# Kernel tuning notes

Hardware: AMD Instinct MI355X
Metric: run time of the kernel (lower is better)

Reference implementation:

```python
import jax, jax.numpy as jnp
import numpy as np


def _prelu(x, a):
    return jnp.where(x >= 0, x, a * x)


def _conv1x1(x, w, b, a):
    # x: [N,C,H,W], w: [O,C], b: [O] -> PReLU(conv1x1(x))
    y = jnp.einsum('oc,nchw->nohw', w, x) + b[None, :, None, None]
    return _prelu(y, a)


def setup_inputs() -> dict:
    key = jax.random.key(0)
    ks = jax.random.split(key, 8)
    N, C, H, W = 4, 128, 64, 64
    Cr = C // 2  # reduction=2
    sC = 1.0 / np.sqrt(C)
    x = jax.random.normal(ks[0], (N, C, H, W), dtype=jnp.float32)
    w1 = jax.random.normal(ks[1], (Cr, C), dtype=jnp.float32) * sC
    b1 = jnp.zeros((Cr,), dtype=jnp.float32)
    a1 = jnp.asarray(0.25, dtype=jnp.float32)  # PReLU (single shared slope)
    w2 = jax.random.normal(ks[2], (Cr, C), dtype=jnp.float32) * sC
    b2 = jnp.zeros((Cr,), dtype=jnp.float32)
    a2 = jnp.asarray(0.25, dtype=jnp.float32)
    wa = jax.random.normal(ks[3], (C, C), dtype=jnp.float32) * sC
    ba = jnp.zeros((C,), dtype=jnp.float32)
    aa = jnp.asarray(0.25, dtype=jnp.float32)
    return {"x": x, "w1": w1, "b1": b1, "a1": a1,
            "w2": w2, "b2": b2, "a2": a2,
            "wa": wa, "ba": ba, "aa": aa}


def reference(x, w1, b1, a1, w2, b2, a2, wa, ba, aa):
    N, C, H, W = x.shape
    HW = H * W
    e1 = _conv1x1(x, w1, b1, a1).reshape(N, -1, HW)   # [N,Cr,HW]
    e2 = _conv1x1(x, w2, b2, a2).reshape(N, -1, HW)   # [N,Cr,HW]
    asm = _conv1x1(x, wa, ba, aa).reshape(N, C, HW)   # [N,C,HW]
    # ksize=1: per-channel outer products summed over channels == single contraction
    score = jnp.einsum('nci,ncj->nij', e1, e2)        # [N,HW,HW]
    score = jax.nn.softmax(score, axis=2)
    out = jnp.einsum('nij,ncj->nci', score, asm)      # [N,C,HW]
    return out.reshape(N, C, H, W)
```

## Files before the change

kernel.cpp:

```cpp
#include <hip/hip_runtime.h>
#include <hip/hip_bf16.h>
#include <stdint.h>


typedef float   f32x16 __attribute__((ext_vector_type(16)));
typedef __bf16  bf16x8 __attribute__((ext_vector_type(8)));
typedef __bf16  bf16x2 __attribute__((ext_vector_type(2)));
typedef unsigned int u32x4 __attribute__((ext_vector_type(4)));
typedef unsigned int u32x2 __attribute__((ext_vector_type(2)));

#define L2E 1.4426950408889634f

#define Q_OFF   (0u)
#define K_OFF   (2u << 20)
#define V_OFF   (4u << 20)
#define DEN_OFF (8u << 20)
#define WH_OFF  ((8u << 20) + (1u << 19))
#define WL_OFF  (WH_OFF + (1u << 16))
#define OP_OFF  (9u << 20)

__device__ inline unsigned short f2bf(float f) {
  unsigned u = __builtin_bit_cast(unsigned, f);
  return (unsigned short)((u + 0x7FFFu + ((u >> 16) & 1u)) >> 16);
}
__device__ inline float bf2f(unsigned short h) {
  unsigned u = ((unsigned)h) << 16;
  return __builtin_bit_cast(float, u);
}

__device__ inline void gld_lds16(const void* g, void* l) {
  __builtin_amdgcn_global_load_lds(
      (const __attribute__((address_space(1))) unsigned*)g,
      (__attribute__((address_space(3))) unsigned*)l, 16, 0, 0);
}

__global__ void wcast_kernel(const float* __restrict__ w1, const float* __restrict__ w2,
                             const float* __restrict__ wa, char* __restrict__ ws) {
  int idx = blockIdx.x * 256 + threadIdx.x;
  unsigned short* WH = (unsigned short*)(ws + WH_OFF);
  unsigned short* WL = (unsigned short*)(ws + WL_OFF);
#pragma unroll
  for (int r = 0; r < 4; ++r) {
    int i = r * 8192 + idx;
    int oc = i >> 7, c = i & 127;
    float v = oc < 64 ? w1[oc * 128 + c]
            : (oc < 128 ? w2[(oc - 64) * 128 + c] : wa[(oc - 128) * 128 + c]);
    unsigned short h = f2bf(v);
    WH[i] = h;
    WL[i] = f2bf(v - bf2f(h));
  }
}

__global__ __launch_bounds__(256) void conv_kernel(
    const float* __restrict__ x, char* __restrict__ ws,
    const float* __restrict__ b1, const float* __restrict__ a1,
    const float* __restrict__ b2, const float* __restrict__ a2,
    const float* __restrict__ ba, const float* __restrict__ aa) {
  int bid = blockIdx.x;
  int n = bid >> 7, st = bid & 127;
  int sb = st * 32;
  int tid = threadIdx.x;
  int wid = tid >> 6, lane = tid & 63, l31 = lane & 31, hi = lane >> 5;

  __shared__ float xl[128][36];
  __shared__ float tl[2][64][33];

  const float* xb = x + (size_t)n * 128 * 4096;
#pragma unroll
  for (int it = 0; it < 4; ++it) {
    int flat4 = tid + 256 * it;
    int c = flat4 >> 3, s4 = flat4 & 7;
    float4 v = *(const float4*)(xb + (size_t)c * 4096 + sb + s4 * 4);
    *(float4*)&xl[c][s4 * 4] = v;
  }
  __syncthreads();

  const char* WH = ws + WH_OFF;
  const char* WL = ws + WL_OFF;
  int oc0 = wid * 64;

  f32x16 acc[2];
  acc[0] = 0.f; acc[1] = 0.f;
#pragma unroll
  for (int c0 = 0; c0 < 8; ++c0) {
    __bf16 eh[8], el[8];
#pragma unroll
    for (int j = 0; j < 8; ++j) {
      float v = xl[c0 * 16 + hi * 8 + j][l31];
      __bf16 h = (__bf16)v;
      eh[j] = h;
      el[j] = (__bf16)(v - (float)h);
    }
    bf16x8 xh = {eh[0], eh[1], eh[2], eh[3], eh[4], eh[5], eh[6], eh[7]};
    bf16x8 xlo = {el[0], el[1], el[2], el[3], el[4], el[5], el[6], el[7]};
#pragma unroll
    for (int mb = 0; mb < 2; ++mb) {
      size_t wo = (size_t)(oc0 + mb * 32 + l31) * 256 + c0 * 32 + hi * 16;
      bf16x8 wh = *(const bf16x8*)(WH + wo);
      bf16x8 wl = *(const bf16x8*)(WL + wo);
      acc[mb] = __builtin_amdgcn_mfma_f32_32x32x16_bf16(wh, xh, acc[mb], 0, 0, 0);
      acc[mb] = __builtin_amdgcn_mfma_f32_32x32x16_bf16(wh, xlo, acc[mb], 0, 0, 0);
      acc[mb] = __builtin_amdgcn_mfma_f32_32x32x16_bf16(wl, xh, acc[mb], 0, 0, 0);
    }
  }

  char* Qw = ws + Q_OFF + (size_t)n * (4096 * 64 * 2);
  char* Kw = ws + K_OFF + (size_t)n * (4096 * 64 * 2);
  unsigned short* Vw = (unsigned short*)(ws + V_OFF) + (size_t)n * 128 * 4096;

  if (wid < 2) {
    const float* bb = wid ? b2 : b1;
    float slope = wid ? a2[0] : a1[0];
    float scl = wid ? 1.0f : L2E;
#pragma unroll
    for (int mb = 0; mb < 2; ++mb)
#pragma unroll
      for (int reg = 0; reg < 16; ++reg) {
        int row = mb * 32 + (reg & 3) + 8 * (reg >> 2) + 4 * hi;
        float y = acc[mb][reg] + bb[row];
        y = fmaxf(y, 0.f) + slope * fminf(y, 0.f);
        tl[wid][row][l31] = y * scl;
      }
  } else {
    float slope = aa[0];
#pragma unroll
    for (int mb = 0; mb < 2; ++mb)
#pragma unroll
      for (int reg = 0; reg < 16; ++reg) {
        int dv = (wid - 2) * 64 + mb * 32 + (reg & 3) + 8 * (reg >> 2) + 4 * hi;
        float y = acc[mb][reg] + ba[dv];
        y = fmaxf(y, 0.f) + slope * fminf(y, 0.f);
        Vw[(size_t)dv * 4096 + sb + l31] = f2bf(y);
      }
  }
  __syncthreads();
  if (wid < 2) {
    char* Og = wid ? Kw : Qw;
#pragma unroll
    for (int it = 0; it < 4; ++it) {
      int sl = (lane >> 3) + it * 8;
      unsigned short u[8];
#pragma unroll
      for (int i = 0; i < 8; ++i) u[i] = f2bf(tl[wid][(lane & 7) * 8 + i][sl]);
      u32x4 pv;
      pv.x = ((unsigned)u[1] << 16) | u[0]; pv.y = ((unsigned)u[3] << 16) | u[2];
      pv.z = ((unsigned)u[5] << 16) | u[4]; pv.w = ((unsigned)u[7] << 16) | u[6];
      *(u32x4*)(Og + (size_t)(sb + sl) * 128 + (lane & 7) * 16) = pv;
    }
  }
}

__global__ __launch_bounds__(256, 4) void attn_kernel(char* __restrict__ ws) {
  int bid = blockIdx.x;
  int split = bid & 7;
  int qt = (bid >> 3) & 31;
  int batch = bid >> 8;
  int tid = threadIdx.x;
  int wid = tid >> 6, lane = tid & 63, l31 = lane & 31, hi = lane >> 5;

  const char* Qb = ws + Q_OFF + (size_t)batch * (4096 * 64 * 2);
  const char* Kb = ws + K_OFF + (size_t)batch * (4096 * 64 * 2);
  const char* Vb = ws + V_OFF + (size_t)batch * (128 * 4096 * 2);

  __shared__ char kbuf[2][32 * 128];
  __shared__ char vbuf[2][128 * 64];

  int q0 = qt * 128 + wid * 32;

  bf16x8 qf[4];
#pragma unroll
  for (int d0 = 0; d0 < 4; ++d0)
    qf[d0] = *(const bf16x8*)(Qb + (size_t)(q0 + l31) * 128 + d0 * 32 + hi * 16);

  f32x16 oacc[4];
#pragma unroll
  for (int i = 0; i < 4; ++i) oacc[i] = 0.f;
  float den = 0.f;

  int t0 = split * 16;

  auto stage = [&](int b, int tile) {
    int kv0 = tile * 32;
    {
      int base = wid * 1024;
      int L = base + (lane << 4);
      int r = L >> 7, sl = (L >> 4) & 7;
      const char* src = Kb + (size_t)(kv0 + r) * 128 + ((sl ^ (r & 7)) << 4);
      gld_lds16(src, &kbuf[b][base]);
    }
#pragma unroll
    for (int i = 0; i < 2; ++i) {
      int base = wid * 2048 + i * 1024;
      int L = base + (lane << 4);
      int r = L >> 6, sl = (L >> 4) & 3;
      const char* src = Vb + (size_t)r * 8192 + kv0 * 2 + ((sl ^ (r & 3)) << 4);
      gld_lds16(src, &vbuf[b][base]);
    }
  };

  stage(0, t0);
  __syncthreads();
  int cur = 0;

  for (int t = 0; t < 16; ++t) {
    if (t + 1 < 16) stage(cur ^ 1, t0 + t + 1);

    f32x16 sacc;
    sacc = 0.f;
    __builtin_amdgcn_s_setprio(1);
#pragma unroll
    for (int d0 = 0; d0 < 4; ++d0) {
      int r = l31;
      bf16x8 kf = *(const bf16x8*)(
          &kbuf[cur][r * 128 + (((d0 * 2 + hi) ^ (r & 7)) << 4)]);
      sacc = __builtin_amdgcn_mfma_f32_32x32x16_bf16(kf, qf[d0], sacc, 0, 0, 0);
    }
    __builtin_amdgcn_s_setprio(0);

    unsigned pk[8];
#pragma unroll
    for (int m = 0; m < 8; ++m) {
      float e0 = __builtin_amdgcn_exp2f(sacc[2 * m]);
      float e1 = __builtin_amdgcn_exp2f(sacc[2 * m + 1]);
      den += e0 + e1;
      bf16x2 bp = { (__bf16)e0, (__bf16)e1 };
      pk[m] = __builtin_bit_cast(unsigned, bp);
    }

#pragma unroll
    for (int kc = 0; kc < 2; ++kc) {
      const int bs = kc * 4;
      u32x2 r0 = __builtin_amdgcn_permlane32_swap(pk[bs + 0], pk[bs + 2],
                                                  false, false);
      u32x2 r1 = __builtin_amdgcn_permlane32_swap(pk[bs + 1], pk[bs + 3],
                                                  false, false);
      u32x4 pu = {r0.x, r1.x, r0.y, r1.y};
      bf16x8 pf = __builtin_bit_cast(bf16x8, pu);
      __builtin_amdgcn_s_setprio(1);
#pragma unroll
      for (int dvb = 0; dvb < 4; ++dvb) {
        int r = dvb * 32 + l31;
        bf16x8 vf = *(const bf16x8*)(
            &vbuf[cur][r * 64 + (((kc * 2 + hi) ^ (r & 3)) << 4)]);
        oacc[dvb] = __builtin_amdgcn_mfma_f32_32x32x16_bf16(vf, pf,
                                                            oacc[dvb], 0, 0, 0);
      }
      __builtin_amdgcn_s_setprio(0);
    }

    __syncthreads();
    cur ^= 1;
  }

  unsigned short* OPu = (unsigned short*)(ws + OP_OFF) +
                        (size_t)((batch * 32 + qt) * 8 + split) * 128 * 128;
  int qloc = wid * 32 + l31;
#pragma unroll
  for (int dvb = 0; dvb < 4; ++dvb)
#pragma unroll
    for (int reg = 0; reg < 16; ++reg) {
      int dv = dvb * 32 + (reg & 3) + 8 * (reg >> 2) + 4 * hi;
      OPu[dv * 128 + qloc] = f2bf(oacc[dvb][reg]);
    }
  float dtot = den + __shfl_xor(den, 32, 64);
  if (hi == 0) {
    float* DEN = (float*)(ws + DEN_OFF) +
                 (size_t)((batch * 32 + qt) * 8 + split) * 128;
    DEN[qloc] = dtot;
  }
}

__global__ __launch_bounds__(256) void combine_kernel(const char* __restrict__ ws,
                                                      float* __restrict__ out) {
  int idx = blockIdx.x * 256 + threadIdx.x;
  int n = idx >> 19;
  int dv = (idx >> 12) & 127;
  int s = idx & 4095;
  int qt = s >> 7, ql = s & 127;
  const unsigned short* OPu = (const unsigned short*)(ws + OP_OFF);
  const float* DEN = (const float*)(ws + DEN_OFF);
  size_t pb = (size_t)((n * 32 + qt) * 8);
  float num = 0.f, den = 0.f;
#pragma unroll
  for (int h = 0; h < 8; ++h) {
    num += bf2f(OPu[(pb + h) * 16384 + (size_t)dv * 128 + ql]);
    den += DEN[(pb + h) * 128 + ql];
  }
  out[idx] = num / den;
}

extern "C" void kernel_launch(void* const* d_in, const int* in_sizes, int n_in,
                              void* d_out, int out_size, void* d_ws, size_t ws_size,
                              hipStream_t stream) {
  (void)in_sizes; (void)n_in; (void)out_size; (void)ws_size;
  const float* x  = (const float*)d_in[0];
  const float* w1 = (const float*)d_in[1];
  const float* b1 = (const float*)d_in[2];
  const float* a1 = (const float*)d_in[3];
  const float* w2 = (const float*)d_in[4];
  const float* b2 = (const float*)d_in[5];
  const float* a2 = (const float*)d_in[6];
  const float* wa = (const float*)d_in[7];
  const float* ba = (const float*)d_in[8];
  const float* aa = (const float*)d_in[9];
  char* ws = (char*)d_ws;
  float* out = (float*)d_out;

  wcast_kernel<<<dim3(32), dim3(256), 0, stream>>>(w1, w2, wa, ws);
  conv_kernel<<<dim3(512), dim3(256), 0, stream>>>(x, ws, b1, a1, b2, a2, ba, aa);
  attn_kernel<<<dim3(1024), dim3(256), 0, stream>>>(ws);
  combine_kernel<<<dim3(8192), dim3(256), 0, stream>>>(ws, out);
}
```

Before: 64.13 us.

## Pre-swizzle K/V into MFMA fragment layout and read directly, doubling query tile

The conv kernel now writes K and V in an MFMA-fragment-ordered layout (V staged through LDS first), so the attention kernel loads fragments straight from global memory with no LDS staging and no per-tile barriers. Each wave now handles two 32-query subtiles, so each K/V fragment is reused across 64 queries and the block count is halved. Launch bounds go down to 2 blocks per CU, and partial outputs use nontemporal stores and loads. The risks are more register pressure and lower occupancy, plus global-load latency that the removed LDS double buffer used to hide.

```diff
diff --git a/kernel.cpp b/kernel.cpp
--- a/kernel.cpp
+++ b/kernel.cpp
@@ -12,8 +12,8 @@
 #define L2E 1.4426950408889634f
 
 #define Q_OFF   (0u)
-#define K_OFF   (2u << 20)
-#define V_OFF   (4u << 20)
+#define KF_OFF  (2u << 20)
+#define VF_OFF  (4u << 20)
 #define DEN_OFF (8u << 20)
 #define WH_OFF  ((8u << 20) + (1u << 19))
 #define WL_OFF  (WH_OFF + (1u << 16))
@@ -26,12 +26,6 @@
 __device__ inline float bf2f(unsigned short h) {
   unsigned u = ((unsigned)h) << 16;
   return __builtin_bit_cast(float, u);
-}
-
-__device__ inline void gld_lds16(const void* g, void* l) {
-  __builtin_amdgcn_global_load_lds(
-      (const __attribute__((address_space(1))) unsigned*)g,
-      (__attribute__((address_space(3))) unsigned*)l, 16, 0, 0);
 }
 
 __global__ void wcast_kernel(const float* __restrict__ w1, const float* __restrict__ w2,
@@ -64,6 +58,7 @@
 
   __shared__ float xl[128][36];
   __shared__ float tl[2][64][33];
+  float* vl = (float*)xl;
 
   const float* xb = x + (size_t)n * 128 * 4096;
 #pragma unroll
@@ -103,10 +98,7 @@
       acc[mb] = __builtin_amdgcn_mfma_f32_32x32x16_bf16(wl, xh, acc[mb], 0, 0, 0);
     }
   }
-
-  char* Qw = ws + Q_OFF + (size_t)n * (4096 * 64 * 2);
-  char* Kw = ws + K_OFF + (size_t)n * (4096 * 64 * 2);
-  unsigned short* Vw = (unsigned short*)(ws + V_OFF) + (size_t)n * 128 * 4096;
+  __syncthreads();
 
   if (wid < 2) {
     const float* bb = wid ? b2 : b1;
@@ -130,143 +122,163 @@
         int dv = (wid - 2) * 64 + mb * 32 + (reg & 3) + 8 * (reg >> 2) + 4 * hi;
         float y = acc[mb][reg] + ba[dv];
         y = fmaxf(y, 0.f) + slope * fminf(y, 0.f);
-        Vw[(size_t)dv * 4096 + sb + l31] = f2bf(y);
+        vl[dv * 33 + l31] = y;
       }
   }
   __syncthreads();
-  if (wid < 2) {
-    char* Og = wid ? Kw : Qw;
+
+  if (wid == 0) {
+    char* Qg = ws + Q_OFF + (size_t)n * (4096 * 128);
 #pragma unroll
     for (int it = 0; it < 4; ++it) {
       int sl = (lane >> 3) + it * 8;
       unsigned short u[8];
 #pragma unroll
-      for (int i = 0; i < 8; ++i) u[i] = f2bf(tl[wid][(lane & 7) * 8 + i][sl]);
+      for (int i = 0; i < 8; ++i) u[i] = f2bf(tl[0][(lane & 7) * 8 + i][sl]);
       u32x4 pv;
       pv.x = ((unsigned)u[1] << 16) | u[0]; pv.y = ((unsigned)u[3] << 16) | u[2];
       pv.z = ((unsigned)u[5] << 16) | u[4]; pv.w = ((unsigned)u[7] << 16) | u[6];
-      *(u32x4*)(Og + (size_t)(sb + sl) * 128 + (lane & 7) * 16) = pv;
-    }
-  }
-}
-
-__global__ __launch_bounds__(256, 4) void attn_kernel(char* __restrict__ ws) {
+      *(u32x4*)(Qg + (size_t)(sb + sl) * 128 + (lane & 7) * 16) = pv;
+    }
+  } else if (wid == 1) {
+    char* KFb = ws + KF_OFF + (size_t)n * (512 << 10);
+    int d0 = (lane & 7) >> 1, hs = lane & 1;
+#pragma unroll
+    for (int it = 0; it < 4; ++it) {
+      int sl = (lane >> 3) + it * 8;
+      unsigned short u[8];
+#pragma unroll
+      for (int i = 0; i < 8; ++i) u[i] = f2bf(tl[1][(lane & 7) * 8 + i][sl]);
+      u32x4 pv;
+      pv.x = ((unsigned)u[1] << 16) | u[0]; pv.y = ((unsigned)u[3] << 16) | u[2];
+      pv.z = ((unsigned)u[5] << 16) | u[4]; pv.w = ((unsigned)u[7] << 16) | u[6];
+      *(u32x4*)(KFb + ((size_t)(st * 4 + d0) * 64 + hs * 32 + sl) * 16) = pv;
+    }
+  }
+  {
+    char* VFb = ws + VF_OFF + (size_t)n * (1u << 20);
+#pragma unroll
+    for (int r = 0; r < 2; ++r) {
+      int u = tid + r * 256;
+      int dv = u >> 2, sc = u & 3;
+      unsigned short b[8];
+#pragma unroll
+      for (int i = 0; i < 8; ++i) b[i] = f2bf(vl[dv * 33 + sc * 8 + i]);
+      u32x4 pv;
+      pv.x = ((unsigned)b[1] << 16) | b[0]; pv.y = ((unsigned)b[3] << 16) | b[2];
+      pv.z = ((unsigned)b[5] << 16) | b[4]; pv.w = ((unsigned)b[7] << 16) | b[6];
+      int unit = st * 8 + (dv >> 5) * 2 + (sc >> 1);
+      *(u32x4*)(VFb + ((size_t)unit * 64 + (sc & 1) * 32 + (dv & 31)) * 16) = pv;
+    }
+  }
+}
+
+__global__ __launch_bounds__(256, 2) void attn_kernel(char* __restrict__ ws) {
   int bid = blockIdx.x;
   int split = bid & 7;
-  int qt = (bid >> 3) & 31;
-  int batch = bid >> 8;
+  int g = bid >> 3;
+  int qt = g & 15;
+  int batch = g >> 4;
   int tid = threadIdx.x;
   int wid = tid >> 6, lane = tid & 63, l31 = lane & 31, hi = lane >> 5;
 
-  const char* Qb = ws + Q_OFF + (size_t)batch * (4096 * 64 * 2);
-  const char* Kb = ws + K_OFF + (size_t)batch * (4096 * 64 * 2);
-  const char* Vb = ws + V_OFF + (size_t)batch * (128 * 4096 * 2);
-
-  __shared__ char kbuf[2][32 * 128];
-  __shared__ char vbuf[2][128 * 64];
-
-  int q0 = qt * 128 + wid * 32;
-
-  bf16x8 qf[4];
-#pragma unroll
-  for (int d0 = 0; d0 < 4; ++d0)
-    qf[d0] = *(const bf16x8*)(Qb + (size_t)(q0 + l31) * 128 + d0 * 32 + hi * 16);
-
-  f32x16 oacc[4];
-#pragma unroll
-  for (int i = 0; i < 4; ++i) oacc[i] = 0.f;
-  float den = 0.f;
-
-  int t0 = split * 16;
-
-  auto stage = [&](int b, int tile) {
-    int kv0 = tile * 32;
-    {
-      int base = wid * 1024;
-      int L = base + (lane << 4);
-      int r = L >> 7, sl = (L >> 4) & 7;
-      const char* src = Kb + (size_t)(kv0 + r) * 128 + ((sl ^ (r & 7)) << 4);
-      gld_lds16(src, &kbuf[b][base]);
-    }
-#pragma unroll
-    for (int i = 0; i < 2; ++i) {
-      int base = wid * 2048 + i * 1024;
-      int L = base + (lane << 4);
-      int r = L >> 6, sl = (L >> 4) & 3;
-      const char* src = Vb + (size_t)r * 8192 + kv0 * 2 + ((sl ^ (r & 3)) << 4);
-      gld_lds16(src, &vbuf[b][base]);
-    }
-  };
-
-  stage(0, t0);
-  __syncthreads();
-  int cur = 0;
-
-  for (int t = 0; t < 16; ++t) {
-    if (t + 1 < 16) stage(cur ^ 1, t0 + t + 1);
-
-    f32x16 sacc;
-    sacc = 0.f;
-    __builtin_amdgcn_s_setprio(1);
-#pragma unroll
-    for (int d0 = 0; d0 < 4; ++d0) {
-      int r = l31;
-      bf16x8 kf = *(const bf16x8*)(
-          &kbuf[cur][r * 128 + (((d0 * 2 + hi) ^ (r & 7)) << 4)]);
-      sacc = __builtin_amdgcn_mfma_f32_32x32x16_bf16(kf, qf[d0], sacc, 0, 0, 0);
-    }
-    __builtin_amdgcn_s_setprio(0);
-
-    unsigned pk[8];
-#pragma unroll
-    for (int m = 0; m < 8; ++m) {
-      float e0 = __builtin_amdgcn_exp2f(sacc[2 * m]);
-      float e1 = __builtin_amdgcn_exp2f(sacc[2 * m + 1]);
-      den += e0 + e1;
-      bf16x2 bp = { (__bf16)e0, (__bf16)e1 };
-      pk[m] = __builtin_bit_cast(unsigned, bp);
+  const char* Qb  = ws + Q_OFF  + (size_t)batch * (4096 * 128);
+  const char* KFb = ws + KF_OFF + (size_t)batch * (512 << 10);
+  const char* VFb = ws + VF_OFF + (size_t)batch * (1u << 20);
+
+  int q0 = qt * 256 + wid * 64;
+
+  bf16x8 qf[2][4];
+#pragma unroll
+  for (int qs = 0; qs < 2; ++qs)
+#pragma unroll
+    for (int d0 = 0; d0 < 4; ++d0)
+      qf[qs][d0] = *(const bf16x8*)(Qb + (size_t)(q0 + qs * 32 + l31) * 128 +
+                                    d0 * 32 + hi * 16);
+
+  f32x16 oacc[2][4];
+#pragma unroll
+  for (int qs = 0; qs < 2; ++qs)
+#pragma unroll
+    for (int i = 0; i < 4; ++i) oacc[qs][i] = 0.f;
+  float den[2] = {0.f, 0.f};
+
+  for (int tt = 0; tt < 16; ++tt) {
+    int t = split * 16 + tt;
+    const char* Kt = KFb + (size_t)t * 4096;
+    const char* Vt = VFb + (size_t)t * 8192;
+
+    bf16x8 kf[4];
+#pragma unroll
+    for (int u = 0; u < 4; ++u)
+      kf[u] = *(const bf16x8*)(Kt + u * 1024 + lane * 16);
+
+    unsigned pk[2][8];
+#pragma unroll
+    for (int qs = 0; qs < 2; ++qs) {
+      f32x16 sacc;
+      sacc = 0.f;
+      __builtin_amdgcn_s_setprio(1);
+#pragma unroll
+      for (int d0 = 0; d0 < 4; ++d0)
+        sacc = __builtin_amdgcn_mfma_f32_32x32x16_bf16(kf[d0], qf[qs][d0],
+                                                       sacc, 0, 0, 0);
+      __builtin_amdgcn_s_setprio(0);
+#pragma unroll
+      for (int m = 0; m < 8; ++m) {
+        float e0 = __builtin_amdgcn_exp2f(sacc[2 * m]);
+        float e1 = __builtin_amdgcn_exp2f(sacc[2 * m + 1]);
+        den[qs] += e0 + e1;
+        bf16x2 bp = { (__bf16)e0, (__bf16)e1 };
+        pk[qs][m] = __builtin_bit_cast(unsigned, bp);
+      }
     }
 
 #pragma unroll
     for (int kc = 0; kc < 2; ++kc) {
       const int bs = kc * 4;
-      u32x2 r0 = __builtin_amdgcn_permlane32_swap(pk[bs + 0], pk[bs + 2],
-                                                  false, false);
-      u32x2 r1 = __builtin_amdgcn_permlane32_swap(pk[bs + 1], pk[bs + 3],
-                                                  false, false);
-      u32x4 pu = {r0.x, r1.x, r0.y, r1.y};
-      bf16x8 pf = __builtin_bit_cast(bf16x8, pu);
+      bf16x8 pf[2];
+#pragma unroll
+      for (int qs = 0; qs < 2; ++qs) {
+        u32x2 r0 = __builtin_amdgcn_permlane32_swap(pk[qs][bs + 0],
+                                                    pk[qs][bs + 2], false, false);
+        u32x2 r1 = __builtin_amdgcn_permlane32_swap(pk[qs][bs + 1],
+                                                    pk[qs][bs + 3], false, false);
+        u32x4 pu = {r0.x, r1.x, r0.y, r1.y};
+        pf[qs] = __builtin_bit_cast(bf16x8, pu);
+      }
       __builtin_amdgcn_s_setprio(1);
 #pragma unroll
       for (int dvb = 0; dvb < 4; ++dvb) {
-        int r = dvb * 32 + l31;
-        bf16x8 vf = *(const bf16x8*)(
-            &vbuf[cur][r * 64 + (((kc * 2 + hi) ^ (r & 3)) << 4)]);
-        oacc[dvb] = __builtin_amdgcn_mfma_f32_32x32x16_bf16(vf, pf,
-                                                            oacc[dvb], 0, 0, 0);
+        bf16x8 vf = *(const bf16x8*)(Vt + (dvb * 2 + kc) * 1024 + lane * 16);
+        oacc[0][dvb] = __builtin_amdgcn_mfma_f32_32x32x16_bf16(vf, pf[0],
+                                                               oacc[0][dvb], 0, 0, 0);
+        oacc[1][dvb] = __builtin_amdgcn_mfma_f32_32x32x16_bf16(vf, pf[1],
+                                                               oacc[1][dvb], 0, 0, 0);
       }
       __builtin_amdgcn_s_setprio(0);
     }
-
-    __syncthreads();
-    cur ^= 1;
   }
 
   unsigned short* OPu = (unsigned short*)(ws + OP_OFF) +
-                        (size_t)((batch * 32 + qt) * 8 + split) * 128 * 128;
-  int qloc = wid * 32 + l31;
-#pragma unroll
-  for (int dvb = 0; dvb < 4; ++dvb)
-#pragma unroll
-    for (int reg = 0; reg < 16; ++reg) {
-      int dv = dvb * 32 + (reg & 3) + 8 * (reg >> 2) + 4 * hi;
-      OPu[dv * 128 + qloc] = f2bf(oacc[dvb][reg]);
-    }
-  float dtot = den + __shfl_xor(den, 32, 64);
-  if (hi == 0) {
-    float* DEN = (float*)(ws + DEN_OFF) +
-                 (size_t)((batch * 32 + qt) * 8 + split) * 128;
-    DEN[qloc] = dtot;
+                        (size_t)((batch * 16 + qt) * 8 + split) * 32768;
+#pragma unroll
+  for (int qs = 0; qs < 2; ++qs) {
+    int qloc = wid * 64 + qs * 32 + l31;
+#pragma unroll
+    for (int dvb = 0; dvb < 4; ++dvb)
+#pragma unroll
+      for (int reg = 0; reg < 16; ++reg) {
+        int dv = dvb * 32 + (reg & 3) + 8 * (reg >> 2) + 4 * hi;
+        __builtin_nontemporal_store(f2bf(oacc[qs][dvb][reg]),
+                                    &OPu[dv * 256 + qloc]);
+      }
+    float dtot = den[qs] + __shfl_xor(den[qs], 32, 64);
+    if (hi == 0) {
+      float* DEN = (float*)(ws + DEN_OFF) +
+                   (size_t)((batch * 16 + qt) * 8 + split) * 256;
+      DEN[qloc] = dtot;
+    }
   }
 }
 
@@ -276,17 +288,18 @@
   int n = idx >> 19;
   int dv = (idx >> 12) & 127;
   int s = idx & 4095;
-  int qt = s >> 7, ql = s & 127;
+  int qt = s >> 8, ql = s & 255;
   const unsigned short* OPu = (const unsigned short*)(ws + OP_OFF);
   const float* DEN = (const float*)(ws + DEN_OFF);
-  size_t pb = (size_t)((n * 32 + qt) * 8);
+  size_t pb = (size_t)((n * 16 + qt) * 8);
   float num = 0.f, den = 0.f;
 #pragma unroll
   for (int h = 0; h < 8; ++h) {
-    num += bf2f(OPu[(pb + h) * 16384 + (size_t)dv * 128 + ql]);
-    den += DEN[(pb + h) * 128 + ql];
-  }
-  out[idx] = num / den;
+    num += bf2f(__builtin_nontemporal_load(
+        &OPu[(pb + h) * 32768 + (size_t)dv * 256 + ql]));
+    den += DEN[(pb + h) * 256 + ql];
+  }
+  __builtin_nontemporal_store(num / den, &out[idx]);
 }
 
 extern "C" void kernel_launch(void* const* d_in, const int* in_sizes, int n_in,
@@ -308,6 +321,6 @@
 
   wcast_kernel<<<dim3(32), dim3(256), 0, stream>>>(w1, w2, wa, ws);
   conv_kernel<<<dim3(512), dim3(256), 0, stream>>>(x, ws, b1, a1, b2, a2, ba, aa);
-  attn_kernel<<<dim3(1024), dim3(256), 0, stream>>>(ws);
+  attn_kernel<<<dim3(512), dim3(256), 0, stream>>>(ws);
   combine_kernel<<<dim3(8192), dim3(256), 0, stream>>>(ws, out);
 }
```

Measured after the change: 79.63 us. +24.2%, slower.
